# Optimization experiments

Hardware: AMD Instinct MI355X
Metric: run time of the kernel (lower is better)

The kernel has to match this reference:

```python
import jax, jax.numpy as jnp
import numpy as np

N, D, C, K, M = 32768, 512, 64, 16, 128
DEPTH = 4            # log2(K): decision-tree depth per codebook
NODES = K - 1        # 15 internal tree nodes per codebook


def _build_selection_matrix():
    # Node i of the binary tree lives at level log2(i+1) and thresholds the
    # level-l selected dimension of its codebook.
    S = np.zeros((C * NODES, C * DEPTH), dtype=np.float32)
    base = np.zeros((NODES, DEPTH), dtype=np.float32)
    for i in range(NODES):
        base[i, int(np.log2(i + 1))] = 1.0
    for c in range(C):
        S[c * NODES:(c + 1) * NODES, c * DEPTH:(c + 1) * DEPTH] = base
    return S


def _build_bit_matrix():
    # Leaf k scores +1/-1 on each of its DEPTH ancestor nodes; the true leaf
    # attains the maximal score DEPTH.
    base = np.zeros((K, NODES), dtype=np.float32)
    for k in range(K):
        for l in range(DEPTH):
            node = (1 << l) - 1 + (k >> (DEPTH - l))   # ancestor at level l
            bit = (k >> (DEPTH - 1 - l)) & 1            # right(1)/left(0)
            base[k, node] = 1.0 if bit else -1.0
    B = np.zeros((C * K, C * NODES), dtype=np.float32)
    for c in range(C):
        B[c * K:(c + 1) * K, c * NODES:(c + 1) * NODES] = base
    return B


def setup_inputs() -> dict:
    key = jax.random.key(0)
    k1, k2, k3, k4 = jax.random.split(key, 4)
    I = jax.random.normal(k1, (N, D), jnp.float32)
    T = jax.random.normal(k2, (C * NODES,), jnp.float32) * 0.1   # thresholds
    L = jax.random.normal(k3, (M, C, K), jnp.float32)            # LUT
    dims = jnp.sort(jax.random.randint(k4, (C * DEPTH,), 0, D))  # selected cols
    S = jnp.asarray(_build_selection_matrix())
    B = jnp.asarray(_build_bit_matrix())
    temp = jnp.ones((1,), jnp.float32)
    return {"I": I, "T": T, "L": L, "S": S, "B": B, "dims": dims, "temp": temp}


def reference(I, T, L, S, B, dims, temp):
    t = temp[0]
    x_sel = I[:, dims]                                  # (N, C*DEPTH) gather
    h = x_sel @ S.T - T                                 # (N, C*NODES)
    tanh_h = jnp.tanh(h / t)
    # straight-through sign: forward sign(h), backward d(tanh(h/t))
    sign_ste = jnp.sign(h) - jax.lax.stop_gradient(tanh_h) + tanh_h
    b = sign_ste @ B.T                                  # (N, C*K) leaf scores
    soft = jax.nn.softmax(b.reshape(-1, C, K) / t, axis=2)
    hard = jax.nn.one_hot(jnp.argmax(soft, axis=2), K, dtype=soft.dtype)
    # straight-through one-hot encoding E: forward hard, backward soft
    E = hard - jax.lax.stop_gradient(soft) + soft       # (N, C, K)
    return jnp.einsum("nck,mck->nm", E, L)              # LUT gather-sum readout
```

## Files before the change

kernel.cpp:

```cpp
#include <hip/hip_runtime.h>

#define N_TOTAL 32768
#define D_DIM   512
#define C_DIM   64
#define K_DIM   16
#define M_DIM   128
#define NODES_  15
#define ROWS    16

typedef unsigned short u16;
typedef unsigned int   u32;

__device__ __forceinline__ u32 f2bf_bits(float f) {
    u32 u = __float_as_uint(f);
    return (u + 0x7FFFu + ((u >> 16) & 1u)) >> 16;
}
__device__ __forceinline__ float bf_lo(u32 u) { return __uint_as_float(u << 16); }
__device__ __forceinline__ float bf_hi(u32 u) { return __uint_as_float(u & 0xFFFF0000u); }

__global__ __launch_bounds__(256) void build_lut_kernel(
    const float* __restrict__ L, u16* __restrict__ LUT)
{
    int idx = blockIdx.x * 256 + threadIdx.x;
    int q  = idx & 15;
    int kk = (idx >> 4) & 255;
    int p  = idx >> 12;
    int c0 = (2 * p) * 16 + (kk & 15);
    int c1 = (2 * p + 1) * 16 + (kk >> 4);
    u32 w[4];
    #pragma unroll
    for (int h = 0; h < 4; ++h) {
        int m0 = q * 8 + 2 * h;
        float a0 = L[m0 * 1024 + c0]       + L[m0 * 1024 + c1];
        float a1 = L[(m0 + 1) * 1024 + c0] + L[(m0 + 1) * 1024 + c1];
        w[h] = f2bf_bits(a0) | (f2bf_bits(a1) << 16);
    }
    *(uint4*)(LUT + (size_t)((p << 8) | kk) * M_DIM + q * 8) =
        make_uint4(w[0], w[1], w[2], w[3]);
}

__global__ __launch_bounds__(256) void codes_kernel(
    const float* __restrict__ I,
    const float* __restrict__ T,
    const int* __restrict__ dims,
    u32* __restrict__ codes)
{
    __shared__ __align__(16) float sI[ROWS * D_DIM];
    __shared__ float sT[C_DIM * NODES_];
    __shared__ int   sDims[C_DIM * 4];
    __shared__ int   sCode[ROWS * 65];

    const int tid = threadIdx.x;
    const int n0  = blockIdx.x * ROWS;

    sDims[tid] = dims[tid];
    for (int j = tid; j < C_DIM * NODES_; j += 256) sT[j] = T[j];

    {
        const float4* src = (const float4*)(I + (size_t)n0 * D_DIM);
        float4* dst = (float4*)sI;
        #pragma unroll
        for (int p = 0; p < 8; ++p)
            dst[p * 256 + tid] = src[p * 256 + tid];
    }
    __syncthreads();

    for (int t = tid; t < ROWS * C_DIM; t += 256) {
        int row = t >> 6;
        int c   = t & 63;
        const float* v = sI + row * D_DIM;
        int node = 0, k = 0;
        #pragma unroll
        for (int l = 0; l < 4; ++l) {
            float h = v[sDims[(c << 2) + l]] - sT[c * NODES_ + node];
            int bit = (h > 0.0f) ? 1 : 0;
            k = (k << 1) | bit;
            node = (node << 1) + 1 + bit;
        }
        sCode[row * 65 + c] = k;
    }
    __syncthreads();

    if (tid < 128) {
        int r = tid >> 3, w = tid & 7;
        const int* sc = sCode + r * 65 + w * 8;
        u32 word = 0;
        #pragma unroll
        for (int j = 0; j < 8; ++j) word |= ((u32)sc[j]) << (4 * j);
        codes[(size_t)(n0 + r) * 8 + w] = word;
    }
}

__global__ __launch_bounds__(256) void accum_kernel(
    const u32* __restrict__ codes,
    const u16* __restrict__ LUT,
    float* __restrict__ out)
{
    __shared__ u32 sC[ROWS * 8];
    const int tid = threadIdx.x;
    const int n0  = blockIdx.x * ROWS;

    if (tid < 128) sC[tid] = codes[(size_t)n0 * 8 + tid];
    __syncthreads();

    const int r = tid >> 4;
    const int q = tid & 15;

    u32 cw[8];
    #pragma unroll
    for (int w = 0; w < 8; ++w) cw[w] = sC[r * 8 + w];

    float4 acc0 = make_float4(0.f, 0.f, 0.f, 0.f);
    float4 acc1 = make_float4(0.f, 0.f, 0.f, 0.f);

    #pragma unroll
    for (int p = 0; p < 32; ++p) {
        u32 kk = (cw[p >> 2] >> ((p & 3) * 8)) & 255u;
        const uint4 v = *(const uint4*)(LUT + (size_t)(((p << 8) | kk) << 7) + (q << 3));
        acc0.x += bf_lo(v.x); acc0.y += bf_hi(v.x);
        acc0.z += bf_lo(v.y); acc0.w += bf_hi(v.y);
        acc1.x += bf_lo(v.z); acc1.y += bf_hi(v.z);
        acc1.z += bf_lo(v.w); acc1.w += bf_hi(v.w);
    }

    float4* o = (float4*)(out + (size_t)(n0 + r) * M_DIM + (q << 3));
    o[0] = acc0;
    o[1] = acc1;
}

extern "C" void kernel_launch(void* const* d_in, const int* in_sizes, int n_in,
                              void* d_out, int out_size, void* d_ws, size_t ws_size,
                              hipStream_t stream) {
    const float* I    = (const float*)d_in[0];
    const float* T    = (const float*)d_in[1];
    const float* L    = (const float*)d_in[2];
    const int*   dims = (const int*)d_in[5];

    u32* codes = (u32*)d_ws;
    u16* LUT   = (u16*)((char*)d_ws + (1 << 20));

    hipLaunchKernelGGL(build_lut_kernel, dim3(512), dim3(256), 0, stream, L, LUT);
    hipLaunchKernelGGL(codes_kernel, dim3(N_TOTAL / ROWS), dim3(256), 0, stream,
                       I, T, dims, codes);
    hipLaunchKernelGGL(accum_kernel, dim3(N_TOTAL / ROWS), dim3(256), 0, stream,
                       codes, LUT, (float*)d_out);
}
```

Measured before the change: 130.1 us.

## Fuse code computation and LUT accumulation; gather selected columns directly from global

Merges the codes and accumulation kernels into one kernel so the packed codes stay in shared memory instead of going through a global workspace, removing a launch. It also stops staging the full 16x512 input tile in shared memory and instead reads only the 256 selected columns per row straight from global memory. This cuts input traffic to just the sectors touched by the selected columns. The price is uncoalesced scattered global loads in the tree traversal.

```diff
diff --git a/kernel.cpp b/kernel.cpp
--- a/kernel.cpp
+++ b/kernel.cpp
@@ -39,13 +39,13 @@
         make_uint4(w[0], w[1], w[2], w[3]);
 }
 
-__global__ __launch_bounds__(256) void codes_kernel(
+__global__ __launch_bounds__(256) void fused_kernel(
     const float* __restrict__ I,
     const float* __restrict__ T,
     const int* __restrict__ dims,
-    u32* __restrict__ codes)
+    const u16* __restrict__ LUT,
+    float* __restrict__ out)
 {
-    __shared__ __align__(16) float sI[ROWS * D_DIM];
     __shared__ float sT[C_DIM * NODES_];
     __shared__ int   sDims[C_DIM * 4];
     __shared__ int   sCode[ROWS * 65];
@@ -55,20 +55,12 @@
 
     sDims[tid] = dims[tid];
     for (int j = tid; j < C_DIM * NODES_; j += 256) sT[j] = T[j];
-
-    {
-        const float4* src = (const float4*)(I + (size_t)n0 * D_DIM);
-        float4* dst = (float4*)sI;
-        #pragma unroll
-        for (int p = 0; p < 8; ++p)
-            dst[p * 256 + tid] = src[p * 256 + tid];
-    }
     __syncthreads();
 
     for (int t = tid; t < ROWS * C_DIM; t += 256) {
         int row = t >> 6;
         int c   = t & 63;
-        const float* v = sI + row * D_DIM;
+        const float* v = I + (size_t)(n0 + row) * D_DIM;
         int node = 0, k = 0;
         #pragma unroll
         for (int l = 0; l < 4; ++l) {
@@ -81,41 +73,16 @@
     }
     __syncthreads();
 
-    if (tid < 128) {
-        int r = tid >> 3, w = tid & 7;
-        const int* sc = sCode + r * 65 + w * 8;
-        u32 word = 0;
-        #pragma unroll
-        for (int j = 0; j < 8; ++j) word |= ((u32)sc[j]) << (4 * j);
-        codes[(size_t)(n0 + r) * 8 + w] = word;
-    }
-}
-
-__global__ __launch_bounds__(256) void accum_kernel(
-    const u32* __restrict__ codes,
-    const u16* __restrict__ LUT,
-    float* __restrict__ out)
-{
-    __shared__ u32 sC[ROWS * 8];
-    const int tid = threadIdx.x;
-    const int n0  = blockIdx.x * ROWS;
-
-    if (tid < 128) sC[tid] = codes[(size_t)n0 * 8 + tid];
-    __syncthreads();
-
     const int r = tid >> 4;
     const int q = tid & 15;
-
-    u32 cw[8];
-    #pragma unroll
-    for (int w = 0; w < 8; ++w) cw[w] = sC[r * 8 + w];
+    const int* codeRow = sCode + r * 65;
 
     float4 acc0 = make_float4(0.f, 0.f, 0.f, 0.f);
     float4 acc1 = make_float4(0.f, 0.f, 0.f, 0.f);
 
     #pragma unroll
     for (int p = 0; p < 32; ++p) {
-        u32 kk = (cw[p >> 2] >> ((p & 3) * 8)) & 255u;
+        u32 kk = (u32)codeRow[2 * p] | ((u32)codeRow[2 * p + 1] << 4);
         const uint4 v = *(const uint4*)(LUT + (size_t)(((p << 8) | kk) << 7) + (q << 3));
         acc0.x += bf_lo(v.x); acc0.y += bf_hi(v.x);
         acc0.z += bf_lo(v.y); acc0.w += bf_hi(v.y);
@@ -136,12 +103,9 @@
     const float* L    = (const float*)d_in[2];
     const int*   dims = (const int*)d_in[5];
 
-    u32* codes = (u32*)d_ws;
-    u16* LUT   = (u16*)((char*)d_ws + (1 << 20));
+    u16* LUT = (u16*)d_ws;
 
     hipLaunchKernelGGL(build_lut_kernel, dim3(512), dim3(256), 0, stream, L, LUT);
-    hipLaunchKernelGGL(codes_kernel, dim3(N_TOTAL / ROWS), dim3(256), 0, stream,
-                       I, T, dims, codes);
-    hipLaunchKernelGGL(accum_kernel, dim3(N_TOTAL / ROWS), dim3(256), 0, stream,
-                       codes, LUT, (float*)d_out);
+    hipLaunchKernelGGL(fused_kernel, dim3(N_TOTAL / ROWS), dim3(256), 0, stream,
+                       I, T, dims, LUT, (float*)d_out);
 }
```

New measurement: 124.8 us. -4.0%, faster.
